# Optimization experiments

Measured on AMD Instinct MI355X. Metric: run time of the kernel, lower is better.

## Reference

```python
import jax, jax.numpy as jnp
import numpy as np

N = 20000   # nodes
E = 320000  # edges (before self loops)
T = 32768   # total tokens for BiLSTM/Transformer features
H = 4       # heads
C = 64      # emb_dim per head
NEG_SLOPE = 0.2


def gat_layer(x, W, a_src, a_dst, b, src, dst):
    # x: [N, Fin] -> h: [N, H, C]
    h = (x @ W).reshape(N, H, C)
    al = jnp.einsum('nhc,hc->nh', h, a_src)  # source attention logits
    ar = jnp.einsum('nhc,hc->nh', h, a_dst)  # target attention logits
    e = jax.nn.leaky_relu(al[src] + ar[dst], NEG_SLOPE)  # [Etot, H]
    m = jax.ops.segment_max(e, dst, num_segments=N)      # [N, H]
    ex = jnp.exp(e - m[dst])
    s = jax.ops.segment_sum(ex, dst, num_segments=N)
    alpha = ex / (s[dst] + 1e-16)                         # edge softmax per target
    msg = alpha[:, :, None] * h[src]                      # [Etot, H, C]
    out = jax.ops.segment_sum(msg, dst, num_segments=N)   # aggr='add'
    return out.reshape(N, H * C) + b


def setup_inputs() -> dict:
    key = jax.random.key(0)
    ks = jax.random.split(key, 32)
    s = 0.05
    rn = lambda k, sh, sc=1.0: jax.random.normal(k, sh, dtype=jnp.float32) * sc
    inp = {}
    inp['x'] = rn(ks[0], (N, 128))
    inp['edge_index'] = jax.random.randint(ks[1], (2, E), 0, N, dtype=jnp.int32)
    inp['batch'] = jnp.sort(jax.random.randint(ks[2], (N,), 0, 64, dtype=jnp.int32))
    inp['VOCindex'] = jnp.sort(jax.random.randint(ks[3], (N,), 0, T, dtype=jnp.int32))
    inp['BiLSTM_feature'] = rn(ks[4], (T, 128))
    inp['Transformer_feature'] = rn(ks[5], (T, 128))
    inp['W0'] = rn(ks[6], (128, H * C), s)
    inp['a_src0'] = rn(ks[7], (H, C), s)
    inp['a_dst0'] = rn(ks[8], (H, C), s)
    inp['b0'] = rn(ks[9], (H * C,), s)
    inp['W1'] = rn(ks[10], (H * C, H * C), s)
    inp['a_src1'] = rn(ks[11], (H, C), s)
    inp['a_dst1'] = rn(ks[12], (H, C), s)
    inp['b1'] = rn(ks[13], (H * C,), s)
    inp['W2'] = rn(ks[14], (H * C, H * C), s)
    inp['a_src2'] = rn(ks[15], (H, C), s)
    inp['a_dst2'] = rn(ks[16], (H, C), s)
    inp['b2'] = rn(ks[17], (H * C,), s)
    inp['fcmax_w'] = rn(ks[18], (H * C, H * C), s)
    inp['fcmax_b'] = rn(ks[19], (H * C,), s)
    inp['fc1_w'] = rn(ks[20], (3 * 2 * H * C, 2 * H * C), s)
    inp['fc1_b'] = rn(ks[21], (2 * H * C,), s)
    inp['fc2_w'] = rn(ks[22], (2 * H * C, 2 * C), s)
    inp['fc2_b'] = rn(ks[23], (2 * C,), s)
    inp['fc3_w'] = rn(ks[24], (2 * C, C), s)
    inp['fc3_b'] = rn(ks[25], (C,), s)
    return inp


def reference(x, edge_index, batch, VOCindex, BiLSTM_feature, Transformer_feature,
              W0, a_src0, a_dst0, b0, W1, a_src1, a_dst1, b1, W2, a_src2, a_dst2, b2,
              fcmax_w, fcmax_b, fc1_w, fc1_b, fc2_w, fc2_b, fc3_w, fc3_b):
    loop = jnp.arange(N, dtype=edge_index.dtype)
    src = jnp.concatenate([edge_index[0], loop])  # PyG GATConv adds self-loops
    dst = jnp.concatenate([edge_index[1], loop])
    params = [(W0, a_src0, a_dst0, b0), (W1, a_src1, a_dst1, b1), (W2, a_src2, a_dst2, b2)]
    h = x
    x_all = []
    for (W, asr, ads, b) in params:
        h = gat_layer(h, W, asr, ads, b, src, dst)
        x_all.append(h)
        h = jax.nn.relu(h @ fcmax_w + fcmax_b)
        x_all.append(h)
    z = jnp.concatenate(x_all, axis=1)               # [N, 1536]
    z = jax.nn.relu(z @ fc1_w + fc1_b)
    z = jax.nn.relu(z @ fc2_w + fc2_b)
    gnn_feature = z @ fc3_w + fc3_b                   # [N, C]
    b_sel = BiLSTM_feature[VOCindex]                  # [N, 128]
    t_sel = Transformer_feature[VOCindex]             # [N, 128]
    return (b_sel, t_sel, gnn_feature, batch)
```

## Files before the change

### kernel.cpp

```cpp
#include <hip/hip_runtime.h>
#include <math.h>

#define NN 20000
#define NPAD 20096
#define EE 320000
#define ET (EE + NN)

typedef __attribute__((ext_vector_type(8))) short bf16x8;
typedef __attribute__((ext_vector_type(4))) float f32x4;
typedef __attribute__((ext_vector_type(4))) unsigned short us4;
typedef __attribute__((ext_vector_type(8))) unsigned short us8;
typedef __attribute__((ext_vector_type(4))) float fx4;

__device__ inline unsigned short f2bf(float f) {
    union { float f; unsigned u; } x; x.f = f;
    unsigned u = x.u;
    return (unsigned short)((u + 0x7FFF + ((u >> 16) & 1)) >> 16);
}
__device__ inline float bf2f(unsigned short u) {
    union { unsigned u; float f; } x; x.u = (unsigned)u << 16; return x.f;
}

__device__ inline void storeC(float* C, size_t idx, float v) { C[idx] = v; }
__device__ inline void storeC(unsigned short* C, size_t idx, float v) { C[idx] = f2bf(v); }

__device__ inline void gload_lds16(const void* g, void* l) {
    __builtin_amdgcn_global_load_lds(
        (const __attribute__((address_space(1))) unsigned int*)g,
        (__attribute__((address_space(3))) unsigned int*)l, 16, 0, 0);
}

__device__ inline int xcd_swz(int orig, int nwg) {
    int q = nwg >> 3, r = nwg & 7;
    int xcd = orig & 7, loc = orig >> 3;
    return (xcd < r ? xcd * (q + 1) : r * (q + 1) + (xcd - r) * q) + loc;
}

__device__ inline void transpose_tile(const float* __restrict__ W, unsigned short* __restrict__ Wt,
                                      int K, int N, int lb) {
    __shared__ float t[32][33];
    int kb = K >> 5;
    int k0 = (lb % kb) * 32, n0 = (lb / kb) * 32;
    int c = threadIdx.x & 31, r8 = threadIdx.x >> 5;
    #pragma unroll
    for (int i = 0; i < 4; i++)
        t[r8 + i * 8][c] = W[(size_t)(k0 + r8 + i * 8) * N + n0 + c];
    __syncthreads();
    #pragma unroll
    for (int i = 0; i < 4; i++)
        Wt[(size_t)(n0 + r8 + i * 8) * K + k0 + c] = f2bf(t[c][r8 + i * 8]);
}

__global__ __launch_bounds__(256) void transpose_all(
    const float* s0, unsigned short* d0,
    const float* s1, unsigned short* d1,
    const float* s2, unsigned short* d2,
    const float* s3, unsigned short* d3,
    const float* s4, unsigned short* d4,
    const float* s5, unsigned short* d5,
    const float* s6, unsigned short* d6)
{
    int b = blockIdx.x;
    if      (b < 32)   transpose_tile(s0, d0, 128, 256, b);
    else if (b < 96)   transpose_tile(s1, d1, 256, 256, b - 32);
    else if (b < 160)  transpose_tile(s2, d2, 256, 256, b - 96);
    else if (b < 224)  transpose_tile(s3, d3, 256, 256, b - 160);
    else if (b < 992)  transpose_tile(s4, d4, 1536, 512, b - 224);
    else if (b < 1056) transpose_tile(s5, d5, 512, 128, b - 992);
    else               transpose_tile(s6, d6, 128, 64, b - 1056);
}

__global__ void cvt_bf16_v4(const float* __restrict__ in, unsigned short* __restrict__ out, int n4) {
    int i = blockIdx.x * blockDim.x + threadIdx.x;
    if (i < n4) {
        fx4 v = *(const fx4*)(in + (size_t)i * 4);
        us4 s;
        #pragma unroll
        for (int j = 0; j < 4; j++) s[j] = f2bf(v[j]);
        *(us4*)(out + (size_t)i * 4) = s;
    }
}

__global__ void count_edges(const int* dst, int* cnt) {
    int e = blockIdx.x * blockDim.x + threadIdx.x;
    if (e < EE) atomicAdd(&cnt[dst[e]], 1);
}

__global__ void scan_kernel(const int* cnt, int* indptr, int* cursor, int* esrc) {
    __shared__ int part[1024];
    int tid = threadIdx.x;
    const int CH = 20;
    int base = tid * CH;
    int sum = 0;
    for (int i = 0; i < CH; i++) {
        int idx = base + i;
        if (idx < NN) sum += cnt[idx] + 1;
    }
    part[tid] = sum;
    __syncthreads();
    for (int off = 1; off < 1024; off <<= 1) {
        int v = (tid >= off) ? part[tid - off] : 0;
        __syncthreads();
        part[tid] += v;
        __syncthreads();
    }
    int run = (tid == 0) ? 0 : part[tid - 1];
    for (int i = 0; i < CH; i++) {
        int idx = base + i;
        if (idx < NN) {
            indptr[idx] = run;
            esrc[run] = idx;
            cursor[idx] = run + 1;
            run += cnt[idx] + 1;
        }
    }
    if (tid == 1023) indptr[NN] = run;
}

__global__ void scatter_edges(const int* src, const int* dst, int* cursor, int* esrc) {
    int e = blockIdx.x * blockDim.x + threadIdx.x;
    if (e < EE) {
        int pos = atomicAdd(&cursor[dst[e]], 1);
        esrc[pos] = src[e];
    }
}

template <int KTOT, typename TC>
__global__ __launch_bounds__(256) void sshot_gemm(
    const unsigned short* __restrict__ A, int lda,
    const unsigned short* __restrict__ Bt, int ldbt,
    TC* __restrict__ C, int ldc,
    int M, const float* __restrict__ bias, int relu, int nwgx)
{
    constexpr int LPR = KTOT / 8;
    constexpr int RPC = 512 / KTOT;
    constexpr int NCH = KTOT / 8;
    constexpr int NCHW = NCH / 4;
    constexpr int KC = KTOT / 32;
    __shared__ unsigned short Als[64 * KTOT];
    __shared__ unsigned short Bls[64 * KTOT];

    int swz = xcd_swz(blockIdx.x, gridDim.x);
    int bx = swz % nwgx, by = swz / nwgx;
    int row0 = by * 64, col0 = bx * 64;

    int tid = threadIdx.x;
    int lane = tid & 63, w = tid >> 6;
    int ric = lane / LPR, slot = lane % LPR;

    #pragma unroll
    for (int i = 0; i < NCHW; i++) {
        int ch = w * NCHW + i;
        int r = ch * RPC + ric;
        gload_lds16(A + (size_t)(row0 + r) * lda + ((slot ^ (r & 7)) << 3),
                    &Als[ch * 512 + lane * 8]);
    }
    #pragma unroll
    for (int i = 0; i < NCHW; i++) {
        int ch = w * NCHW + i;
        int r = ch * RPC + ric;
        gload_lds16(Bt + (size_t)(col0 + r) * ldbt + ((slot ^ (r & 7)) << 3),
                    &Bls[ch * 512 + lane * 8]);
    }
    __syncthreads();

    f32x4 acc[4];
    #pragma unroll
    for (int j = 0; j < 4; j++) acc[j] = (f32x4){0.f, 0.f, 0.f, 0.f};

    #pragma unroll
    for (int kc = 0; kc < KC; kc++) {
        int ks = (kc << 2) + (lane >> 4);
        int ra = (w << 4) + (lane & 15);
        bf16x8 af = *(bf16x8*)&Als[ra * KTOT + ((ks ^ (ra & 7)) << 3)];
        #pragma unroll
        for (int j = 0; j < 4; j++) {
            int rb = (j << 4) + (lane & 15);
            bf16x8 bf = *(bf16x8*)&Bls[rb * KTOT + ((ks ^ (rb & 7)) << 3)];
            acc[j] = __builtin_amdgcn_mfma_f32_16x16x32_bf16(af, bf, acc[j], 0, 0, 0);
        }
    }

    #pragma unroll
    for (int rr = 0; rr < 4; rr++) {
        int row = row0 + (w << 4) + ((lane >> 4) << 2) + rr;
        if (row >= M) continue;
        #pragma unroll
        for (int j = 0; j < 4; j++) {
            int col = col0 + j * 16 + (lane & 15);
            float v = acc[j][rr] + (bias ? bias[col] : 0.f);
            if (relu) v = fmaxf(v, 0.f);
            storeC(C, (size_t)row * ldc + col, v);
        }
    }
}

template <int BN, typename TC, bool LOGITS>
__global__ __launch_bounds__(256) void mfma_gemm(
    const unsigned short* __restrict__ A, int lda,
    const unsigned short* __restrict__ Bt, int ldbt,
    TC* __restrict__ C, int ldc,
    int M, int K,
    const float* __restrict__ bias, int relu, int nwgx,
    const float* __restrict__ asrc, const float* __restrict__ adst,
    float* __restrict__ al, float* __restrict__ ar)
{
    constexpr int BM = 128, BK = 64;
    constexpr int WNW = (BN >= 128) ? 2 : 1;
    constexpr int WMW = 4 / WNW;
    constexpr int RW = BM / WMW;
    constexpr int NI = RW / 16;
    constexpr int NJ = 4;
    constexpr int NCHB = BN / 8;
    constexpr int PER_STAGE = 4 + NCHB / 4;
    __shared__ unsigned short Als[2][BM * BK];
    __shared__ unsigned short Bls[2][BN * BK];

    int swz = xcd_swz(blockIdx.x, gridDim.x);
    int bx = swz % nwgx, by = swz / nwgx;

    int tid = threadIdx.x;
    int lane = tid & 63, w = tid >> 6;
    int wm = (WNW == 2) ? (w >> 1) : w;
    int wn = (WNW == 2) ? (w & 1) : 0;
    int row0 = by * BM, col0 = bx * BN;

    int lr = lane >> 3;
    int scol = ((lane & 7) ^ lr) << 3;

    f32x4 acc[NI][NJ];
    #pragma unroll
    for (int i = 0; i < NI; i++)
        #pragma unroll
        for (int j = 0; j < NJ; j++) acc[i][j] = (f32x4){0.f, 0.f, 0.f, 0.f};

    auto stage = [&](int buf, int k0) {
        #pragma unroll
        for (int i = 0; i < 4; i++) {
            int ch = (w << 2) + i;
            gload_lds16(A + (size_t)(row0 + (ch << 3) + lr) * lda + k0 + scol,
                        &Als[buf][(ch << 9) + (lane << 3)]);
        }
        #pragma unroll
        for (int i = 0; i < NCHB / 4; i++) {
            int ch = w * (NCHB / 4) + i;
            gload_lds16(Bt + (size_t)(col0 + (ch << 3) + lr) * ldbt + k0 + scol,
                        &Bls[buf][(ch << 9) + (lane << 3)]);
        }
    };

    auto compute = [&](int buf) {
        #pragma unroll
        for (int kc = 0; kc < 2; kc++) {
            int ks = (kc << 2) + (lane >> 4);
            bf16x8 af[NI];
            #pragma unroll
            for (int i = 0; i < NI; i++) {
                int rr = wm * RW + (i << 4) + (lane & 15);
                af[i] = *(bf16x8*)&Als[buf][(rr << 6) + ((ks ^ (rr & 7)) << 3)];
            }
            bf16x8 bfr[NJ];
            #pragma unroll
            for (int j = 0; j < NJ; j++) {
                int rr = wn * 64 + (j << 4) + (lane & 15);
                bfr[j] = *(bf16x8*)&Bls[buf][(rr << 6) + ((ks ^ (rr & 7)) << 3)];
            }
            #pragma unroll
            for (int i = 0; i < NI; i++)
                #pragma unroll
                for (int j = 0; j < NJ; j++)
                    acc[i][j] = __builtin_amdgcn_mfma_f32_16x16x32_bf16(af[i], bfr[j], acc[i][j], 0, 0, 0);
        }
    };

    int NT = K >> 6;
    stage(0, 0);
    stage(1, BK);
    for (int t = 0; t < NT; ++t) {
        if (t < NT - 1)
            asm volatile("s_waitcnt vmcnt(%0)" :: "i"(PER_STAGE) : "memory");
        else
            asm volatile("s_waitcnt vmcnt(0)" ::: "memory");
        __builtin_amdgcn_s_barrier();
        compute(t & 1);
        if (t + 2 < NT) {
            __builtin_amdgcn_s_barrier();
            stage(t & 1, (t + 2) << 6);
        }
    }

    if constexpr (LOGITS) {
        int hh = col0 >> 6;
        float as_j[NJ], ad_j[NJ];
        #pragma unroll
        for (int j = 0; j < NJ; j++) {
            int cl = j * 16 + (lane & 15);
            as_j[j] = asrc[hh * 64 + cl];
            ad_j[j] = adst[hh * 64 + cl];
        }
        #pragma unroll
        for (int i = 0; i < NI; i++) {
            #pragma unroll
            for (int rr = 0; rr < 4; rr++) {
                int row = row0 + wm * RW + (i << 4) + ((lane >> 4) << 2) + rr;
                float ps = 0.f, pd = 0.f;
                #pragma unroll
                for (int j = 0; j < NJ; j++) {
                    float v = acc[i][j][rr];
                    ps += v * as_j[j];
                    pd += v * ad_j[j];
                    if (row < M) {
                        int col = col0 + j * 16 + (lane & 15);
                        storeC(C, (size_t)row * ldc + col, v);
                    }
                }
                #pragma unroll
                for (int off = 8; off; off >>= 1) {
                    ps += __shfl_xor(ps, off);
                    pd += __shfl_xor(pd, off);
                }
                if ((lane & 15) == 0 && row < M) {
                    al[row * 4 + hh] = ps;
                    ar[row * 4 + hh] = pd;
                }
            }
        }
    } else {
        #pragma unroll
        for (int i = 0; i < NI; i++) {
            #pragma unroll
            for (int rr = 0; rr < 4; rr++) {
                int row = row0 + wm * RW + (i << 4) + ((lane >> 4) << 2) + rr;
                if (row >= M) continue;
                #pragma unroll
                for (int j = 0; j < NJ; j++) {
                    int col = col0 + wn * 64 + j * 16 + (lane & 15);
                    float v = acc[i][j][rr] + (bias ? bias[col] : 0.f);
                    if (relu) v = fmaxf(v, 0.f);
                    storeC(C, (size_t)row * ldc + col, v);
                }
            }
        }
    }
}

__global__ __launch_bounds__(256) void aggregate_kernel(
    const unsigned short* __restrict__ hbuf,
    const float* __restrict__ al, const float* __restrict__ ar,
    const int* __restrict__ indptr, const int* __restrict__ esrc,
    const float* __restrict__ bias,
    unsigned short* __restrict__ out, int ldo)
{
    int w = threadIdx.x >> 6;
    int n = blockIdx.x * 4 + w;
    if (n >= NN) return;
    int lane = threadIdx.x & 63;
    int myh = lane >> 4;
    int c4 = lane * 4;
    int beg = indptr[n], end = indptr[n + 1];

    float arh = ar[(size_t)n * 4 + myh];

    float ssum = 0.f;
    fx4 acc = (fx4){0.f, 0.f, 0.f, 0.f};
    int j = beg;
    for (; j + 4 <= end; j += 4) {
        int s0 = esrc[j], s1 = esrc[j + 1], s2 = esrc[j + 2], s3 = esrc[j + 3];
        us4 h0 = *(const us4*)&hbuf[(size_t)s0 * 256 + c4];
        us4 h1 = *(const us4*)&hbuf[(size_t)s1 * 256 + c4];
        us4 h2 = *(const us4*)&hbuf[(size_t)s2 * 256 + c4];
        us4 h3 = *(const us4*)&hbuf[(size_t)s3 * 256 + c4];
        float a0 = al[(size_t)s0 * 4 + myh];
        float a1 = al[(size_t)s1 * 4 + myh];
        float a2 = al[(size_t)s2 * 4 + myh];
        float a3 = al[(size_t)s3 * 4 + myh];
        float e0 = a0 + arh; e0 = e0 > 0.f ? e0 : 0.2f * e0;
        float e1 = a1 + arh; e1 = e1 > 0.f ? e1 : 0.2f * e1;
        float e2 = a2 + arh; e2 = e2 > 0.f ? e2 : 0.2f * e2;
        float e3 = a3 + arh; e3 = e3 > 0.f ? e3 : 0.2f * e3;
        float x0 = __expf(e0), x1 = __expf(e1);
        float x2 = __expf(e2), x3 = __expf(e3);
        ssum += x0 + x1 + x2 + x3;
        #pragma unroll
        for (int k = 0; k < 4; k++)
            acc[k] += x0 * bf2f(h0[k]) + x1 * bf2f(h1[k])
                    + x2 * bf2f(h2[k]) + x3 * bf2f(h3[k]);
    }
    for (; j < end; j++) {
        int s = esrc[j];
        us4 hv = *(const us4*)&hbuf[(size_t)s * 256 + c4];
        float a = al[(size_t)s * 4 + myh];
        float e = a + arh; e = e > 0.f ? e : 0.2f * e;
        float ex = __expf(e);
        ssum += ex;
        #pragma unroll
        for (int k = 0; k < 4; k++) acc[k] += ex * bf2f(hv[k]);
    }

    float inv = 1.f / (ssum + 1e-16f);
    us4 o;
    #pragma unroll
    for (int k = 0; k < 4; k++) o[k] = f2bf(acc[k] * inv + bias[c4 + k]);
    *(us4*)&out[(size_t)n * ldo + c4] = o;
}

__global__ void gather_feats(const float* __restrict__ Bf, const float* __restrict__ Tf,
                             const int* __restrict__ voc, const int* __restrict__ batch,
                             float* __restrict__ out)
{
    int i = blockIdx.x * blockDim.x + threadIdx.x;
    if (i < NN * 32) {
        int n = i >> 5, c4 = (i & 31) * 4;
        int t = voc[n];
        *(fx4*)&out[(size_t)n * 128 + c4] = *(const fx4*)&Bf[(size_t)t * 128 + c4];
        *(fx4*)&out[(size_t)NN * 128 + (size_t)n * 128 + c4] = *(const fx4*)&Tf[(size_t)t * 128 + c4];
    }
    if (i < NN) out[(size_t)NN * 128 * 2 + (size_t)NN * 64 + i] = (float)batch[i];
}

extern "C" void kernel_launch(void* const* d_in, const int* in_sizes, int n_in,
                              void* d_out, int out_size, void* d_ws, size_t ws_size,
                              hipStream_t stream) {
    const float* x     = (const float*)d_in[0];
    const int*   ei    = (const int*)d_in[1];
    const int*   batch = (const int*)d_in[2];
    const int*   voc   = (const int*)d_in[3];
    const float* Bf    = (const float*)d_in[4];
    const float* Tf    = (const float*)d_in[5];
    const float* W0    = (const float*)d_in[6];
    const float* as0   = (const float*)d_in[7];
    const float* ad0   = (const float*)d_in[8];
    const float* b0    = (const float*)d_in[9];
    const float* W1    = (const float*)d_in[10];
    const float* as1   = (const float*)d_in[11];
    const float* ad1   = (const float*)d_in[12];
    const float* b1    = (const float*)d_in[13];
    const float* W2    = (const float*)d_in[14];
    const float* as2   = (const float*)d_in[15];
    const float* ad2   = (const float*)d_in[16];
    const float* b2    = (const float*)d_in[17];
    const float* fcmax_w = (const float*)d_in[18];
    const float* fcmax_b = (const float*)d_in[19];
    const float* fc1_w = (const float*)d_in[20];
    const float* fc1_b = (const float*)d_in[21];
    const float* fc2_w = (const float*)d_in[22];
    const float* fc2_b = (const float*)d_in[23];
    const float* fc3_w = (const float*)d_in[24];
    const float* fc3_b = (const float*)d_in[25];
    float* out = (float*)d_out;

    char* p = (char*)d_ws;
    unsigned short* xb  = (unsigned short*)p; p += (size_t)NPAD * 128 * 2;
    unsigned short* hbuf= (unsigned short*)p; p += (size_t)NN * 256 * 2;
    unsigned short* z   = (unsigned short*)p; p += (size_t)NPAD * 1536 * 2;
    unsigned short* z1  = (unsigned short*)p; p += (size_t)NPAD * 512 * 2;
    unsigned short* h2  = (unsigned short*)p; p += (size_t)NPAD * 128 * 2;
    unsigned short* w0t = (unsigned short*)p; p += (size_t)128 * 256 * 2;
    unsigned short* w1t = (unsigned short*)p; p += (size_t)256 * 256 * 2;
    unsigned short* w2t = (unsigned short*)p; p += (size_t)256 * 256 * 2;
    unsigned short* wmt = (unsigned short*)p; p += (size_t)256 * 256 * 2;
    unsigned short* f1t = (unsigned short*)p; p += (size_t)1536 * 512 * 2;
    unsigned short* f2t = (unsigned short*)p; p += (size_t)512 * 128 * 2;
    unsigned short* f3t = (unsigned short*)p; p += (size_t)128 * 64 * 2;
    float* al   = (float*)p; p += (size_t)NN * 4 * 4;
    float* ar   = (float*)p; p += (size_t)NN * 4 * 4;
    int* cnt    = (int*)p;   p += (size_t)NN * 4;
    int* cursor = (int*)p;   p += (size_t)NN * 4;
    int* esrc   = (int*)p;   p += (size_t)ET * 4;
    int* indptr = (int*)p;   p += (size_t)(NN + 1) * 4;

    const int* e_src = ei;
    const int* e_dst = ei + EE;

    transpose_all<<<1064, 256, 0, stream>>>(W0, w0t, W1, w1t, W2, w2t, fcmax_w, wmt,
                                            fc1_w, f1t, fc2_w, f2t, fc3_w, f3t);
    cvt_bf16_v4<<<(NN * 32 + 255) / 256, 256, 0, stream>>>(x, xb, NN * 32);

    hipMemsetAsync(cnt, 0, (size_t)NN * 4, stream);
    count_edges<<<(EE + 255) / 256, 256, 0, stream>>>(e_dst, cnt);
    scan_kernel<<<1, 1024, 0, stream>>>(cnt, indptr, cursor, esrc);
    scatter_edges<<<(EE + 255) / 256, 256, 0, stream>>>(e_src, e_dst, cursor, esrc);

    gather_feats<<<(NN * 32 + 255) / 256, 256, 0, stream>>>(Bf, Tf, voc, batch, out);

    const int MB = NPAD / 128;
    const int SB = NPAD / 64;
    const int NB4 = (NN + 3) / 4;

    mfma_gemm<64, unsigned short, true><<<4 * MB, 256, 0, stream>>>(xb, 128, w0t, 128, hbuf, 256, NN, 128, nullptr, 0, 4, as0, ad0, al, ar);
    aggregate_kernel<<<NB4, 256, 0, stream>>>(hbuf, al, ar, indptr, esrc, b0, z + 0, 1536);
    mfma_gemm<64, unsigned short, false><<<4 * MB, 256, 0, stream>>>(z + 0, 1536, wmt, 256, z + 256, 1536, NN, 256, fcmax_b, 1, 4, nullptr, nullptr, nullptr, nullptr);

    mfma_gemm<64, unsigned short, true><<<4 * MB, 256, 0, stream>>>(z + 256, 1536, w1t, 256, hbuf, 256, NN, 256, nullptr, 0, 4, as1, ad1, al, ar);
    aggregate_kernel<<<NB4, 256, 0, stream>>>(hbuf, al, ar, indptr, esrc, b1, z + 512, 1536);
    mfma_gemm<64, unsigned short, false><<<4 * MB, 256, 0, stream>>>(z + 512, 1536, wmt, 256, z + 768, 1536, NN, 256, fcmax_b, 1, 4, nullptr, nullptr, nullptr, nullptr);

    mfma_gemm<64, unsigned short, true><<<4 * MB, 256, 0, stream>>>(z + 768, 1536, w2t, 256, hbuf, 256, NN, 256, nullptr, 0, 4, as2, ad2, al, ar);
    aggregate_kernel<<<NB4, 256, 0, stream>>>(hbuf, al, ar, indptr, esrc, b2, z + 1024, 1536);
    mfma_gemm<64, unsigned short, false><<<4 * MB, 256, 0, stream>>>(z + 1024, 1536, wmt, 256, z + 1280, 1536, NN, 256, fcmax_b, 1, 4, nullptr, nullptr, nullptr, nullptr);

    mfma_gemm<64, unsigned short, false><<<8 * MB, 256, 0, stream>>>(z, 1536, f1t, 1536, z1, 512, NN, 1536, fc1_b, 1, 8, nullptr, nullptr, nullptr, nullptr);
    mfma_gemm<64, unsigned short, false><<<2 * MB, 256, 0, stream>>>(z1, 512, f2t, 512, h2, 128, NN, 512, fc2_b, 1, 2, nullptr, nullptr, nullptr, nullptr);
    sshot_gemm<128, float><<<1 * SB, 256, 0, stream>>>(h2, 128, f3t, 128, out + (size_t)2 * NN * 128, 64, NN, fc3_b, 0, 1);
}
```

Baseline: 320.3 us.

## Add 128x128 double-buffered MFMA GEMM kernel for fc1 layer

Adds a dedicated GEMM kernel with 128x128 output tiles, a BK=32 K-step, a two-stage LDS double buffer fed by direct global-to-LDS loads, and a 2x2 wave layout where each wave computes a 4x4 grid of 16x16 MFMA tiles. It replaces the previous 128x64-tile launch for the large fc1 GEMM (K=1536, N=512), halving the grid. The aim is more operand reuse per LDS load and overlap of global loads with MFMA work on the largest GEMM. In exchange it uses more accumulator registers per thread and launches fewer workgroups, which may reduce occupancy.

```diff
diff --git a/kernel.cpp b/kernel.cpp
--- a/kernel.cpp
+++ b/kernel.cpp
@@ -191,6 +191,99 @@
             float v = acc[j][rr] + (bias ? bias[col] : 0.f);
             if (relu) v = fmaxf(v, 0.f);
             storeC(C, (size_t)row * ldc + col, v);
+        }
+    }
+}
+
+__global__ __launch_bounds__(256) void mfma_gemm32(
+    const unsigned short* __restrict__ A, int lda,
+    const unsigned short* __restrict__ Bt, int ldbt,
+    unsigned short* __restrict__ C, int ldc,
+    int M, int K, const float* __restrict__ bias, int nwgx)
+{
+    __shared__ unsigned short Als[2][128 * 32];
+    __shared__ unsigned short Bls[2][128 * 32];
+
+    int swz = xcd_swz(blockIdx.x, gridDim.x);
+    int bx = swz % nwgx, by = swz / nwgx;
+    int tid = threadIdx.x, lane = tid & 63, w = tid >> 6;
+    int wm = w >> 1, wn = w & 1;
+    int row0 = by * 128, col0 = bx * 128;
+
+    int ric = lane >> 2;
+    int scol = ((lane & 3) ^ ((ric >> 1) & 3)) << 3;
+
+    f32x4 acc[4][4];
+    #pragma unroll
+    for (int i = 0; i < 4; i++)
+        #pragma unroll
+        for (int j = 0; j < 4; j++) acc[i][j] = (f32x4){0.f, 0.f, 0.f, 0.f};
+
+    auto stage = [&](int buf, int k0) {
+        #pragma unroll
+        for (int i = 0; i < 2; i++) {
+            int ch = w * 2 + i;
+            int r = (ch << 4) + ric;
+            gload_lds16(A + (size_t)(row0 + r) * lda + k0 + scol,
+                        &Als[buf][(ch << 9) + (lane << 3)]);
+        }
+        #pragma unroll
+        for (int i = 0; i < 2; i++) {
+            int ch = w * 2 + i;
+            int r = (ch << 4) + ric;
+            gload_lds16(Bt + (size_t)(col0 + r) * ldbt + k0 + scol,
+                        &Bls[buf][(ch << 9) + (lane << 3)]);
+        }
+    };
+
+    auto compute = [&](int buf) {
+        int ks = lane >> 4;
+        bf16x8 af[4], bfr[4];
+        #pragma unroll
+        for (int i = 0; i < 4; i++) {
+            int rr = wm * 64 + (i << 4) + (lane & 15);
+            af[i] = *(bf16x8*)&Als[buf][(rr << 5) + ((ks ^ ((rr >> 1) & 3)) << 3)];
+        }
+        #pragma unroll
+        for (int j = 0; j < 4; j++) {
+            int rr = wn * 64 + (j << 4) + (lane & 15);
+            bfr[j] = *(bf16x8*)&Bls[buf][(rr << 5) + ((ks ^ ((rr >> 1) & 3)) << 3)];
+        }
+        #pragma unroll
+        for (int i = 0; i < 4; i++)
+            #pragma unroll
+            for (int j = 0; j < 4; j++)
+                acc[i][j] = __builtin_amdgcn_mfma_f32_16x16x32_bf16(af[i], bfr[j], acc[i][j], 0, 0, 0);
+    };
+
+    int NT = K >> 5;
+    stage(0, 0);
+    stage(1, 32);
+    for (int t = 0; t < NT; ++t) {
+        if (t < NT - 1)
+            asm volatile("s_waitcnt vmcnt(4)" ::: "memory");
+        else
+            asm volatile("s_waitcnt vmcnt(0)" ::: "memory");
+        __builtin_amdgcn_s_barrier();
+        compute(t & 1);
+        if (t + 2 < NT) {
+            __builtin_amdgcn_s_barrier();
+            stage(t & 1, (t + 2) << 5);
+        }
+    }
+
+    #pragma unroll
+    for (int i = 0; i < 4; i++) {
+        #pragma unroll
+        for (int rr = 0; rr < 4; rr++) {
+            int row = row0 + wm * 64 + (i << 4) + ((lane >> 4) << 2) + rr;
+            if (row >= M) continue;
+            #pragma unroll
+            for (int j = 0; j < 4; j++) {
+                int col = col0 + wn * 64 + j * 16 + (lane & 15);
+                float v = fmaxf(acc[i][j][rr] + bias[col], 0.f);
+                C[(size_t)row * ldc + col] = f2bf(v);
+            }
         }
     }
 }
@@ -499,7 +592,7 @@
     aggregate_kernel<<<NB4, 256, 0, stream>>>(hbuf, al, ar, indptr, esrc, b2, z + 1024, 1536);
     mfma_gemm<64, unsigned short, false><<<4 * MB, 256, 0, stream>>>(z + 1024, 1536, wmt, 256, z + 1280, 1536, NN, 256, fcmax_b, 1, 4, nullptr, nullptr, nullptr, nullptr);
 
-    mfma_gemm<64, unsigned short, false><<<8 * MB, 256, 0, stream>>>(z, 1536, f1t, 1536, z1, 512, NN, 1536, fc1_b, 1, 8, nullptr, nullptr, nullptr, nullptr);
+    mfma_gemm32<<<4 * MB, 256, 0, stream>>>(z, 1536, f1t, 1536, z1, 512, NN, 1536, fc1_b, 4);
     mfma_gemm<64, unsigned short, false><<<2 * MB, 256, 0, stream>>>(z1, 512, f2t, 512, h2, 128, NN, 512, fc2_b, 1, 2, nullptr, nullptr, nullptr, nullptr);
     sshot_gemm<128, float><<<1 * SB, 256, 0, stream>>>(h2, 128, f3t, 128, out + (size_t)2 * NN * 128, 64, NN, fc3_b, 0, 1);
 }
```

Result: no change. 316.9 us (-1.1%).
